# Optimization experiments

Hardware: AMD Instinct MI355X
Metric: run time of the kernel (lower is better)

## Reference

```python
import jax, jax.numpy as jnp
import numpy as np

A = 0.7071067811865476  # sqrt(2)/2
B_ = 1.0 - A
KH = KW = 3
K2 = 9
STRIDE = 1
PAD = 1
DIL = 1


def setup_inputs() -> dict:
    key = jax.random.key(0)
    k1, k2, k3, k4 = jax.random.split(key, 4)
    Bn, Cin, H, W = 4, 256, 64, 64
    Cout = 256
    x = jax.random.normal(k1, (Bn, Cin, H, W), dtype=jnp.float32)
    offset = jax.random.normal(k2, (Bn, 2 * K2, H, W), dtype=jnp.float32)
    mask = jax.random.uniform(k3, (Bn, K2, H, W), dtype=jnp.float32)
    stdv = 1.0 / np.sqrt(Cin * KH * KW)
    weight = jax.random.uniform(k4, (Cout, Cin, KH, KW), dtype=jnp.float32,
                                minval=-stdv, maxval=stdv)
    bias = jnp.zeros((Cout,), dtype=jnp.float32)
    return {"input": x, "offset": offset, "mask": mask, "weight": weight, "bias": bias}


def _weight_circle(weight):
    # Blend 3x3 corner taps along the diagonal "circle", as in DCNv2_Circle.forward.
    O, C = weight.shape[0], weight.shape[1]
    w = weight.reshape(O, C, K2)
    w0 = A * (A * w[:, :, 0] + B_ * w[:, :, 1]) + B_ * (A * w[:, :, 3] + B_ * w[:, :, 4])
    w2 = A * (B_ * w[:, :, 1] + A * w[:, :, 2]) + B_ * (B_ * w[:, :, 4] + A * w[:, :, 5])
    w6 = B_ * (A * w[:, :, 3] + B_ * w[:, :, 4]) + A * (A * w[:, :, 6] + B_ * w[:, :, 7])
    w8 = B_ * (B_ * w[:, :, 4] + A * w[:, :, 5]) + A * (B_ * w[:, :, 7] + A * w[:, :, 8])
    return jnp.stack([w0, w[:, :, 1], w2, w[:, :, 3], w[:, :, 4],
                      w[:, :, 5], w6, w[:, :, 7], w8], axis=-1)  # [O, C, 9]


def _dcn_v2(x, offset, mask, w_flat, bias):
    Bn, C, H, W = x.shape
    Ho = (H + 2 * PAD - DIL * (KH - 1) - 1) // STRIDE + 1
    Wo = (W + 2 * PAD - DIL * (KW - 1) - 1) // STRIDE + 1
    # Base sampling grid per kernel tap k: [K2, Ho, Wo]
    ki, kj = jnp.meshgrid(jnp.arange(KH), jnp.arange(KW), indexing="ij")
    ki = ki.reshape(K2).astype(jnp.float32)
    kj = kj.reshape(K2).astype(jnp.float32)
    oy = (jnp.arange(Ho, dtype=jnp.float32) * STRIDE - PAD)
    ox = (jnp.arange(Wo, dtype=jnp.float32) * STRIDE - PAD)
    base_y = oy[None, :, None] + DIL * ki[:, None, None]  # [K2, Ho, 1]
    base_x = ox[None, None, :] + DIL * kj[:, None, None]  # [K2, 1, Wo]
    # Offsets: channel 2k is dy, 2k+1 is dx (DCNv2 layout).
    off = offset.reshape(Bn, K2, 2, Ho, Wo)
    y = base_y[None] + off[:, :, 0]  # [B, K2, Ho, Wo]
    x_ = base_x[None] + off[:, :, 1]
    y0 = jnp.floor(y)
    x0 = jnp.floor(x_)
    ly = y - y0
    lx = x_ - x0
    y0i = y0.astype(jnp.int32)
    x0i = x0.astype(jnp.int32)
    flat = x.reshape(Bn, C, H * W)

    def gather(yi, xi):
        valid = (yi >= 0) & (yi < H) & (xi >= 0) & (xi < W)
        idx = jnp.clip(yi, 0, H - 1) * W + jnp.clip(xi, 0, W - 1)  # [B,K2,Ho,Wo]
        v = jax.vmap(lambda f, i: f[:, i.reshape(-1)])(flat, idx)  # [B,C,K2*Ho*Wo]
        v = v.reshape(Bn, C, K2, Ho, Wo)
        return v * valid[:, None].astype(v.dtype)

    hy = 1.0 - ly
    hx = 1.0 - lx
    # corner weights broadcast over channel dim
    sampled = (gather(y0i, x0i) * (hy * hx)[:, None]
               + gather(y0i, x0i + 1) * (hy * lx)[:, None]
               + gather(y0i + 1, x0i) * (ly * hx)[:, None]
               + gather(y0i + 1, x0i + 1) * (ly * lx)[:, None])  # [B,C,K2,Ho,Wo]
    sampled = sampled * mask[:, None]  # modulation
    out = jnp.einsum("bckhw,ock->bohw", sampled, w_flat)
    return out + bias[None, :, None, None]


def reference(input, offset, mask, weight, bias):
    w_flat = _weight_circle(weight)
    return _dcn_v2(input, offset, mask, w_flat, bias)
```

## Files before the change

kernel.cpp:

```cpp
#include <hip/hip_runtime.h>

typedef __bf16 bf16x8 __attribute__((ext_vector_type(8)));
typedef float f32x4 __attribute__((ext_vector_type(4)));

#define HH 64
#define WW 64
#define HW 4096
#define COUT 256
#define NROWS 12
#define XS_OFF 37888
#define SMEM_SZ 65536

__device__ __forceinline__ void bar_sync() {
    asm volatile("s_waitcnt lgkmcnt(0)" ::: "memory");
    __builtin_amdgcn_s_barrier();
    asm volatile("" ::: "memory");
}
__device__ __forceinline__ void bar_sync_vm() {
    asm volatile("s_waitcnt vmcnt(0) lgkmcnt(0)" ::: "memory");
    __builtin_amdgcn_s_barrier();
    asm volatile("" ::: "memory");
}

__global__ __launch_bounds__(256) void prep_weights(const float* __restrict__ weight,
                                                    __bf16* __restrict__ wp) {
    __shared__ float ws[2304];
    const int o = blockIdx.x;
    const int tid = threadIdx.x;
    const float4* src = (const float4*)(weight + (size_t)o * 2304);
    float4* dst = (float4*)ws;
    #pragma unroll
    for (int i = 0; i < 3; ++i) {
        int idx = i * 256 + tid;
        if (idx < 576) dst[idx] = src[idx];
    }
    __syncthreads();
    const float Af = 0.70710678118654752f;
    const float Bf = 1.0f - Af;
    const int tm = o >> 4, rr = o & 15;
    for (int fid = tid; fid < 288; fid += 256) {
        const int cgtap = fid >> 2, q = fid & 3;
        const int cg = cgtap / 9, tap = cgtap - 9 * cg;
        const int c0 = cg * 32 + q * 8;
        bf16x8 v;
        #pragma unroll
        for (int j = 0; j < 8; ++j) {
            const float* w = ws + (c0 + j) * 9;
            float r;
            switch (tap) {
                case 0:  r = Af*(Af*w[0]+Bf*w[1]) + Bf*(Af*w[3]+Bf*w[4]); break;
                case 1:  r = w[1]; break;
                case 2:  r = Af*(Bf*w[1]+Af*w[2]) + Bf*(Bf*w[4]+Af*w[5]); break;
                case 3:  r = w[3]; break;
                case 4:  r = w[4]; break;
                case 5:  r = w[5]; break;
                case 6:  r = Bf*(Af*w[3]+Bf*w[4]) + Af*(Af*w[6]+Bf*w[7]); break;
                case 7:  r = w[7]; break;
                default: r = Bf*(Bf*w[4]+Af*w[5]) + Af*(Bf*w[7]+Af*w[8]); break;
            }
            v[j] = (__bf16)r;
        }
        *(bf16x8*)&wp[(size_t)(((cg * 9 + tap) * 16 + tm) * 64 + q * 16 + rr) << 3] = v;
    }
}

__global__ __launch_bounds__(256) void prep_x(const float* __restrict__ x,
                                              __bf16* __restrict__ xs) {
    __shared__ float lds[16384];
    const int bh = blockIdx.x;
    const int tid = threadIdx.x;
    const int b = bh >> 6, h = bh & 63;
    const int w4 = (tid & 15) * 4;
    const int cb = tid >> 4;
    #pragma unroll
    for (int it = 0; it < 16; ++it) {
        const int c = cb + it * 16;
        float4 v = *(const float4*)(x + ((size_t)(b * 256 + c)) * HW + h * 64 + w4);
        #pragma unroll
        for (int e = 0; e < 4; ++e) {
            int w = w4 + e;
            lds[w * 256 + (c ^ (w & 31))] = ((const float*)&v)[e];
        }
    }
    __syncthreads();
    #pragma unroll
    for (int it = 0; it < 8; ++it) {
        const int u = it * 256 + tid;
        const int gsg = u >> 6, w = u & 63;
        bf16x8 v;
        #pragma unroll
        for (int c8 = 0; c8 < 8; ++c8)
            v[c8] = (__bf16)lds[w * 256 + ((gsg * 8 + c8) ^ (w & 31))];
        *(bf16x8*)&xs[(size_t)bh * 16384 + (size_t)u * 8] = v;
    }
}

__global__ __launch_bounds__(512, 2) void dcn_main(
        const float* __restrict__ x, const float* __restrict__ off,
        const float* __restrict__ msk, const __bf16* __restrict__ wp,
        const __bf16* __restrict__ xs, const float* __restrict__ bias,
        float* __restrict__ out) {
    __shared__ __align__(16) char smem[SMEM_SZ];
    char* BsB = smem;
    const char* XsB = (const char*)smem + XS_OFF;

    const int tid  = threadIdx.x;
    const int wv   = tid >> 6;
    const int lane = tid & 63;
    const int q    = lane >> 4, rr = lane & 15;
    const int px   = lane;

    const int bid = blockIdx.x;
    const int xcd = bid & 7;
    const int b   = xcd >> 1;
    const int h   = ((xcd & 1) << 5) | (bid >> 3);

    const int rowbase = min(max(h - 5, 0), HH - NROWS);
    const float* xb = x + (size_t)b * 256 * HW;
    const char* xsb = (const char*)xs;

    size_t SB[3]; int XD[3];
    #pragma unroll
    for (int k = 0; k < 3; ++k) {
        int t = wv * 3 + k;
        int row = t >> 1, sgh = t & 1;
        SB[k] = (size_t)(b * 64 + rowbase + row) * 32768 + (size_t)(sgh * 1024 + lane * 16);
        XD[k] = XS_OFF + row * 2048 + sgh * 1024;
    }

    float W00[3], W01[3], W10[3], W11[3];
    int AY0[3], AY1[3], DXO[3], COLB[3], GP[3];
    bool UV[3];
    #pragma unroll
    for (int k = 0; k < 3; ++k) {
        int c = (k < 2) ? (wv + 8 * k) : ((wv >= 6) ? wv + 10 : -1);
        UV[k] = (c >= 0);
        if (UV[k]) {
            int sg = c / 9, tap = c % 9;
            int ki = tap / 3, kj = tap - 3 * ki;
            const float* offp = off + (size_t)b * 18 * HW + h * 64 + px;
            float dy = offp[(2 * tap) * HW];
            float dx = offp[(2 * tap + 1) * HW];
            float mv = msk[(size_t)b * 9 * HW + (size_t)tap * HW + h * 64 + px];
            float py  = (float)(h - 1 + ki) + dy;
            float pxf = (float)(px - 1 + kj) + dx;
            float y0f = floorf(py), x0f = floorf(pxf);
            float ly = py - y0f, lx = pxf - x0f;
            float hy = 1.0f - ly, hx = 1.0f - lx;
            int y0 = (int)y0f, x0 = (int)x0f;
            int y1 = y0 + 1, x1 = x0 + 1;
            bool vy0 = (y0 >= 0) && (y0 < HH), vy1 = (y1 >= 0) && (y1 < HH);
            bool vx0 = (x0 >= 0) && (x0 < WW), vx1 = (x1 >= 0) && (x1 < WW);
            int cy0 = min(max(y0, 0), HH - 1), cy1 = min(max(y1, 0), HH - 1);
            int cx0 = min(max(x0, 0), WW - 1), cx1 = min(max(x1, 0), WW - 1);
            W00[k] = (vy0 && vx0) ? hy * hx * mv : 0.0f;
            W01[k] = (vy0 && vx1) ? hy * lx * mv : 0.0f;
            W10[k] = (vy1 && vx0) ? ly * hx * mv : 0.0f;
            W11[k] = (vy1 && vx1) ? ly * lx * mv : 0.0f;
            int ry0 = min(max(cy0 - rowbase, 0), NROWS - 1);
            int ry1 = min(max(cy1 - rowbase, 0), NROWS - 1);
            bool useG = (vy0 && (cy0 < rowbase || cy0 > rowbase + NROWS - 1))
                     || (vy1 && (cy1 < rowbase || cy1 > rowbase + NROWS - 1));
            AY0[k]  = ry0 * 2048 + sg * 1024 + cx0 * 16;
            AY1[k]  = ry1 * 2048 + sg * 1024 + cx0 * 16;
            DXO[k]  = (cx1 - cx0) * 16;
            COLB[k] = (tap * 32 + sg * 8) * 2;
            GP[k]   = cy0 | (cy1 << 6) | (cx0 << 12) | (cx1 << 18) | (sg << 24)
                    | (useG ? (1u << 31) : 0);
        }
    }

    f32x4 acc[4][4];
    #pragma unroll
    for (int i = 0; i < 4; ++i)
        #pragma unroll
        for (int n = 0; n < 4; ++n)
            acc[i][n] = (f32x4)0.0f;

    const int tm0   = (wv & 3) * 4;
    const int klbeg = (wv & 4) ? 5 : 0;
    const int nkl   = (wv & 4) ? 4 : 5;

    #pragma unroll
    for (int k = 0; k < 3; ++k)
        __builtin_amdgcn_global_load_lds(
            (const __attribute__((address_space(1))) void*)(xsb + SB[k]),
            (__attribute__((address_space(3))) void*)(smem + XD[k]), 16, 0, 0);

    #pragma unroll 1
    for (int s = 0; s < 16; ++s) {
        const int cg = s >> 1, half = s & 1;
        bar_sync_vm();
        #pragma unroll
        for (int k = 0; k < 3; ++k) {
            if (UV[k]) {
                bf16x8 c00 = *(const bf16x8*)(XsB + AY0[k]);
                bf16x8 c01 = *(const bf16x8*)(XsB + AY0[k] + DXO[k]);
                bf16x8 c10 = *(const bf16x8*)(XsB + AY1[k]);
                bf16x8 c11 = *(const bf16x8*)(XsB + AY1[k] + DXO[k]);
                float w0 = W00[k], w1 = W01[k], w2 = W10[k], w3 = W11[k];
                bf16x8 res;
                #pragma unroll
                for (int j = 0; j < 8; ++j) {
                    float v = w0 * (float)c00[j] + w1 * (float)c01[j]
                            + w2 * (float)c10[j] + w3 * (float)c11[j];
                    res[j] = (__bf16)v;
                }
                int gp = GP[k];
                if (gp < 0) {
                    int cy0 = gp & 63, cy1 = (gp >> 6) & 63;
                    int cx0 = (gp >> 12) & 63, cx1 = (gp >> 18) & 63;
                    int sg = (gp >> 24) & 3;
                    const float* xc = xb + (size_t)(cg * 32 + half * 16 + sg * 8) * HW;
                    int i00 = cy0 * 64 + cx0, i01 = cy0 * 64 + cx1;
                    int i10 = cy1 * 64 + cx0, i11 = cy1 * 64 + cx1;
                    #pragma unroll
                    for (int j = 0; j < 8; ++j) {
                        float v = w0 * xc[i00] + w1 * xc[i01]
                                + w2 * xc[i10] + w3 * xc[i11];
                        res[j] = (__bf16)v;
                        xc += HW;
                    }
                }
                *(bf16x8*)(BsB + px * 592 + COLB[k] + half * 32) = res;
            }
        }
        bar_sync();
        if (s < 15) {
            #pragma unroll
            for (int k = 0; k < 3; ++k)
                __builtin_amdgcn_global_load_lds(
                    (const __attribute__((address_space(1))) void*)(xsb + SB[k] + (size_t)(s + 1) * 2048),
                    (__attribute__((address_space(3))) void*)(smem + XD[k]), 16, 0, 0);
        }
        if (half) {
            const __bf16* ap = wp + ((size_t)((cg * 9 + klbeg) * 16 + tm0) * 64 + lane) * 8;
            bf16x8 a0 = *(const bf16x8*)ap;
            bf16x8 a1 = *(const bf16x8*)(ap + 512);
            bf16x8 a2 = *(const bf16x8*)(ap + 1024);
            bf16x8 a3 = *(const bf16x8*)(ap + 1536);
            int kc = (klbeg * 32 + q * 8) * 2;
            #pragma unroll 1
            for (int t = 0; t < nkl; ++t) {
                bf16x8 n0 = a0, n1 = a1, n2 = a2, n3 = a3;
                if (t + 1 < nkl) {
                    const __bf16* np = ap + 8192;
                    n0 = *(const bf16x8*)np;
                    n1 = *(const bf16x8*)(np + 512);
                    n2 = *(const bf16x8*)(np + 1024);
                    n3 = *(const bf16x8*)(np + 1536);
                }
                const char* bp = BsB + rr * 592 + kc;
                bf16x8 bb0 = *(const bf16x8*)(bp);
                bf16x8 bb1 = *(const bf16x8*)(bp + 16 * 592);
                bf16x8 bb2 = *(const bf16x8*)(bp + 32 * 592);
                bf16x8 bb3 = *(const bf16x8*)(bp + 48 * 592);
                acc[0][0] = __builtin_amdgcn_mfma_f32_16x16x32_bf16(a0, bb0, acc[0][0], 0, 0, 0);
                acc[1][0] = __builtin_amdgcn_mfma_f32_16x16x32_bf16(a1, bb0, acc[1][0], 0, 0, 0);
                acc[2][0] = __builtin_amdgcn_mfma_f32_16x16x32_bf16(a2, bb0, acc[2][0], 0, 0, 0);
                acc[3][0] = __builtin_amdgcn_mfma_f32_16x16x32_bf16(a3, bb0, acc[3][0], 0, 0, 0);
                acc[0][1] = __builtin_amdgcn_mfma_f32_16x16x32_bf16(a0, bb1, acc[0][1], 0, 0, 0);
                acc[1][1] = __builtin_amdgcn_mfma_f32_16x16x32_bf16(a1, bb1, acc[1][1], 0, 0, 0);
                acc[2][1] = __builtin_amdgcn_mfma_f32_16x16x32_bf16(a2, bb1, acc[2][1], 0, 0, 0);
                acc[3][1] = __builtin_amdgcn_mfma_f32_16x16x32_bf16(a3, bb1, acc[3][1], 0, 0, 0);
                acc[0][2] = __builtin_amdgcn_mfma_f32_16x16x32_bf16(a0, bb2, acc[0][2], 0, 0, 0);
                acc[1][2] = __builtin_amdgcn_mfma_f32_16x16x32_bf16(a1, bb2, acc[1][2], 0, 0, 0);
                acc[2][2] = __builtin_amdgcn_mfma_f32_16x16x32_bf16(a2, bb2, acc[2][2], 0, 0, 0);
                acc[3][2] = __builtin_amdgcn_mfma_f32_16x16x32_bf16(a3, bb2, acc[3][2], 0, 0, 0);
                acc[0][3] = __builtin_amdgcn_mfma_f32_16x16x32_bf16(a0, bb3, acc[0][3], 0, 0, 0);
                acc[1][3] = __builtin_amdgcn_mfma_f32_16x16x32_bf16(a1, bb3, acc[1][3], 0, 0, 0);
                acc[2][3] = __builtin_amdgcn_mfma_f32_16x16x32_bf16(a2, bb3, acc[2][3], 0, 0, 0);
                acc[3][3] = __builtin_amdgcn_mfma_f32_16x16x32_bf16(a3, bb3, acc[3][3], 0, 0, 0);
                ap += 8192;
                kc += 64;
                a0 = n0; a1 = n1; a2 = n2; a3 = n3;
            }
        }
    }

    float* scr = (float*)smem;
    bar_sync();
    if (wv >= 4) {
        const int base = (wv - 4) * 4096 + lane * 4;
        #pragma unroll
        for (int i = 0; i < 4; ++i)
            #pragma unroll
            for (int n = 0; n < 4; ++n)
                *(f32x4*)&scr[base + (i * 4 + n) * 256] = acc[i][n];
    }
    bar_sync();
    if (wv < 4) {
        const int mrow = wv * 64;
        const int base = wv * 4096 + lane * 4;
        #pragma unroll
        for (int i = 0; i < 4; ++i) {
            #pragma unroll
            for (int n = 0; n < 4; ++n) {
                f32x4 p = *(const f32x4*)&scr[base + (i * 4 + n) * 256];
                #pragma unroll
                for (int e = 0; e < 4; ++e) {
                    int m = mrow + i * 16 + q * 4 + e;
                    out[((size_t)b * COUT + m) * HW + h * 64 + n * 16 + rr]
                        = acc[i][n][e] + p[e] + bias[m];
                }
            }
        }
    }
}

extern "C" void kernel_launch(void* const* d_in, const int* in_sizes, int n_in,
                              void* d_out, int out_size, void* d_ws, size_t ws_size,
                              hipStream_t stream) {
    const float* x      = (const float*)d_in[0];
    const float* off    = (const float*)d_in[1];
    const float* msk    = (const float*)d_in[2];
    const float* weight = (const float*)d_in[3];
    const float* bias   = (const float*)d_in[4];
    float* out = (float*)d_out;

    __bf16* wp = (__bf16*)d_ws;
    __bf16* xs = (__bf16*)((char*)d_ws + 1179648);

    prep_weights<<<256, 256, 0, stream>>>(weight, wp);
    prep_x<<<256, 256, 0, stream>>>(x, xs);
    dcn_main<<<256, 512, 0, stream>>>(x, off, msk, wp, xs, bias, out);
}
```

Baseline: 133.3 us.

## Merge prep kernels and prefetch weight fragments one stage ahead of MFMA

Combines the weight-prep and x-prep kernels into one launch with 512 blocks. The x transpose now reads global memory directly instead of going through an LDS transpose. In the main kernel, the A (weight) fragments for a whole channel group are loaded into registers during the even half-step, so their latency overlaps the bilinear sampling. The MFMA loop is fully unrolled. This saves a launch and hides global-load latency, at the cost of many more VGPRs (20 bf16x8 fragments) under launch_bounds(512,2), which risks spills. The x-prep reads are now strided and uncoalesced.

```diff
diff --git a/kernel.cpp b/kernel.cpp
--- a/kernel.cpp
+++ b/kernel.cpp
@@ -22,11 +22,29 @@
     asm volatile("" ::: "memory");
 }
 
-__global__ __launch_bounds__(256) void prep_weights(const float* __restrict__ weight,
-                                                    __bf16* __restrict__ wp) {
+__global__ __launch_bounds__(256) void prep(const float* __restrict__ weight,
+                                            const float* __restrict__ x,
+                                            __bf16* __restrict__ wp,
+                                            __bf16* __restrict__ xs) {
     __shared__ float ws[2304];
-    const int o = blockIdx.x;
     const int tid = threadIdx.x;
+    if (blockIdx.x < 256) {
+        const int bh = blockIdx.x;
+        const int b = bh >> 6, h = bh & 63;
+        const float* xr = x + (size_t)b * 256 * HW + h * 64;
+        #pragma unroll
+        for (int it = 0; it < 8; ++it) {
+            const int u = it * 256 + tid;
+            const int gsg = u >> 6, w = u & 63;
+            bf16x8 v;
+            #pragma unroll
+            for (int c8 = 0; c8 < 8; ++c8)
+                v[c8] = (__bf16)xr[(size_t)(gsg * 8 + c8) * HW + w];
+            *(bf16x8*)&xs[(size_t)bh * 16384 + (size_t)u * 8] = v;
+        }
+        return;
+    }
+    const int o = blockIdx.x - 256;
     const float4* src = (const float4*)(weight + (size_t)o * 2304);
     float4* dst = (float4*)ws;
     #pragma unroll
@@ -61,37 +79,6 @@
             v[j] = (__bf16)r;
         }
         *(bf16x8*)&wp[(size_t)(((cg * 9 + tap) * 16 + tm) * 64 + q * 16 + rr) << 3] = v;
-    }
-}
-
-__global__ __launch_bounds__(256) void prep_x(const float* __restrict__ x,
-                                              __bf16* __restrict__ xs) {
-    __shared__ float lds[16384];
-    const int bh = blockIdx.x;
-    const int tid = threadIdx.x;
-    const int b = bh >> 6, h = bh & 63;
-    const int w4 = (tid & 15) * 4;
-    const int cb = tid >> 4;
-    #pragma unroll
-    for (int it = 0; it < 16; ++it) {
-        const int c = cb + it * 16;
-        float4 v = *(const float4*)(x + ((size_t)(b * 256 + c)) * HW + h * 64 + w4);
-        #pragma unroll
-        for (int e = 0; e < 4; ++e) {
-            int w = w4 + e;
-            lds[w * 256 + (c ^ (w & 31))] = ((const float*)&v)[e];
-        }
-    }
-    __syncthreads();
-    #pragma unroll
-    for (int it = 0; it < 8; ++it) {
-        const int u = it * 256 + tid;
-        const int gsg = u >> 6, w = u & 63;
-        bf16x8 v;
-        #pragma unroll
-        for (int c8 = 0; c8 < 8; ++c8)
-            v[c8] = (__bf16)lds[w * 256 + ((gsg * 8 + c8) ^ (w & 31))];
-        *(bf16x8*)&xs[(size_t)bh * 16384 + (size_t)u * 8] = v;
     }
 }
 
@@ -181,6 +168,8 @@
     const int klbeg = (wv & 4) ? 5 : 0;
     const int nkl   = (wv & 4) ? 4 : 5;
 
+    bf16x8 Afr[5][4];
+
     #pragma unroll
     for (int k = 0; k < 3; ++k)
         __builtin_amdgcn_global_load_lds(
@@ -191,6 +180,17 @@
     for (int s = 0; s < 16; ++s) {
         const int cg = s >> 1, half = s & 1;
         bar_sync_vm();
+        if (!half) {
+            const __bf16* ap = wp + ((size_t)((cg * 9 + klbeg) * 16 + tm0) * 64 + lane) * 8;
+            #pragma unroll
+            for (int t = 0; t < 5; ++t) {
+                if (t < nkl) {
+                    #pragma unroll
+                    for (int i = 0; i < 4; ++i)
+                        Afr[t][i] = *(const bf16x8*)(ap + t * 8192 + i * 512);
+                }
+            }
+        }
         #pragma unroll
         for (int k = 0; k < 3; ++k) {
             if (UV[k]) {
@@ -234,46 +234,32 @@
                     (__attribute__((address_space(3))) void*)(smem + XD[k]), 16, 0, 0);
         }
         if (half) {
-            const __bf16* ap = wp + ((size_t)((cg * 9 + klbeg) * 16 + tm0) * 64 + lane) * 8;
-            bf16x8 a0 = *(const bf16x8*)ap;
-            bf16x8 a1 = *(const bf16x8*)(ap + 512);
-            bf16x8 a2 = *(const bf16x8*)(ap + 1024);
-            bf16x8 a3 = *(const bf16x8*)(ap + 1536);
-            int kc = (klbeg * 32 + q * 8) * 2;
-            #pragma unroll 1
-            for (int t = 0; t < nkl; ++t) {
-                bf16x8 n0 = a0, n1 = a1, n2 = a2, n3 = a3;
-                if (t + 1 < nkl) {
-                    const __bf16* np = ap + 8192;
-                    n0 = *(const bf16x8*)np;
-                    n1 = *(const bf16x8*)(np + 512);
-                    n2 = *(const bf16x8*)(np + 1024);
-                    n3 = *(const bf16x8*)(np + 1536);
-                }
-                const char* bp = BsB + rr * 592 + kc;
-                bf16x8 bb0 = *(const bf16x8*)(bp);
-                bf16x8 bb1 = *(const bf16x8*)(bp + 16 * 592);
-                bf16x8 bb2 = *(const bf16x8*)(bp + 32 * 592);
-                bf16x8 bb3 = *(const bf16x8*)(bp + 48 * 592);
-                acc[0][0] = __builtin_amdgcn_mfma_f32_16x16x32_bf16(a0, bb0, acc[0][0], 0, 0, 0);
-                acc[1][0] = __builtin_amdgcn_mfma_f32_16x16x32_bf16(a1, bb0, acc[1][0], 0, 0, 0);
-                acc[2][0] = __builtin_amdgcn_mfma_f32_16x16x32_bf16(a2, bb0, acc[2][0], 0, 0, 0);
-                acc[3][0] = __builtin_amdgcn_mfma_f32_16x16x32_bf16(a3, bb0, acc[3][0], 0, 0, 0);
-                acc[0][1] = __builtin_amdgcn_mfma_f32_16x16x32_bf16(a0, bb1, acc[0][1], 0, 0, 0);
-                acc[1][1] = __builtin_amdgcn_mfma_f32_16x16x32_bf16(a1, bb1, acc[1][1], 0, 0, 0);
-                acc[2][1] = __builtin_amdgcn_mfma_f32_16x16x32_bf16(a2, bb1, acc[2][1], 0, 0, 0);
-                acc[3][1] = __builtin_amdgcn_mfma_f32_16x16x32_bf16(a3, bb1, acc[3][1], 0, 0, 0);
-                acc[0][2] = __builtin_amdgcn_mfma_f32_16x16x32_bf16(a0, bb2, acc[0][2], 0, 0, 0);
-                acc[1][2] = __builtin_amdgcn_mfma_f32_16x16x32_bf16(a1, bb2, acc[1][2], 0, 0, 0);
-                acc[2][2] = __builtin_amdgcn_mfma_f32_16x16x32_bf16(a2, bb2, acc[2][2], 0, 0, 0);
-                acc[3][2] = __builtin_amdgcn_mfma_f32_16x16x32_bf16(a3, bb2, acc[3][2], 0, 0, 0);
-                acc[0][3] = __builtin_amdgcn_mfma_f32_16x16x32_bf16(a0, bb3, acc[0][3], 0, 0, 0);
-                acc[1][3] = __builtin_amdgcn_mfma_f32_16x16x32_bf16(a1, bb3, acc[1][3], 0, 0, 0);
-                acc[2][3] = __builtin_amdgcn_mfma_f32_16x16x32_bf16(a2, bb3, acc[2][3], 0, 0, 0);
-                acc[3][3] = __builtin_amdgcn_mfma_f32_16x16x32_bf16(a3, bb3, acc[3][3], 0, 0, 0);
-                ap += 8192;
-                kc += 64;
-                a0 = n0; a1 = n1; a2 = n2; a3 = n3;
+            const char* bp0 = BsB + rr * 592 + (klbeg * 32 + q * 8) * 2;
+            #pragma unroll
+            for (int t = 0; t < 5; ++t) {
+                if (t < nkl) {
+                    const char* bp = bp0 + t * 64;
+                    bf16x8 bb0 = *(const bf16x8*)(bp);
+                    bf16x8 bb1 = *(const bf16x8*)(bp + 16 * 592);
+                    bf16x8 bb2 = *(const bf16x8*)(bp + 32 * 592);
+                    bf16x8 bb3 = *(const bf16x8*)(bp + 48 * 592);
+                    acc[0][0] = __builtin_amdgcn_mfma_f32_16x16x32_bf16(Afr[t][0], bb0, acc[0][0], 0, 0, 0);
+                    acc[1][0] = __builtin_amdgcn_mfma_f32_16x16x32_bf16(Afr[t][1], bb0, acc[1][0], 0, 0, 0);
+                    acc[2][0] = __builtin_amdgcn_mfma_f32_16x16x32_bf16(Afr[t][2], bb0, acc[2][0], 0, 0, 0);
+                    acc[3][0] = __builtin_amdgcn_mfma_f32_16x16x32_bf16(Afr[t][3], bb0, acc[3][0], 0, 0, 0);
+                    acc[0][1] = __builtin_amdgcn_mfma_f32_16x16x32_bf16(Afr[t][0], bb1, acc[0][1], 0, 0, 0);
+                    acc[1][1] = __builtin_amdgcn_mfma_f32_16x16x32_bf16(Afr[t][1], bb1, acc[1][1], 0, 0, 0);
+                    acc[2][1] = __builtin_amdgcn_mfma_f32_16x16x32_bf16(Afr[t][2], bb1, acc[2][1], 0, 0, 0);
+                    acc[3][1] = __builtin_amdgcn_mfma_f32_16x16x32_bf16(Afr[t][3], bb1, acc[3][1], 0, 0, 0);
+                    acc[0][2] = __builtin_amdgcn_mfma_f32_16x16x32_bf16(Afr[t][0], bb2, acc[0][2], 0, 0, 0);
+                    acc[1][2] = __builtin_amdgcn_mfma_f32_16x16x32_bf16(Afr[t][1], bb2, acc[1][2], 0, 0, 0);
+                    acc[2][2] = __builtin_amdgcn_mfma_f32_16x16x32_bf16(Afr[t][2], bb2, acc[2][2], 0, 0, 0);
+                    acc[3][2] = __builtin_amdgcn_mfma_f32_16x16x32_bf16(Afr[t][3], bb2, acc[3][2], 0, 0, 0);
+                    acc[0][3] = __builtin_amdgcn_mfma_f32_16x16x32_bf16(Afr[t][0], bb3, acc[0][3], 0, 0, 0);
+                    acc[1][3] = __builtin_amdgcn_mfma_f32_16x16x32_bf16(Afr[t][1], bb3, acc[1][3], 0, 0, 0);
+                    acc[2][3] = __builtin_amdgcn_mfma_f32_16x16x32_bf16(Afr[t][2], bb3, acc[2][3], 0, 0, 0);
+                    acc[3][3] = __builtin_amdgcn_mfma_f32_16x16x32_bf16(Afr[t][3], bb3, acc[3][3], 0, 0, 0);
+                }
             }
         }
     }
@@ -321,7 +307,6 @@
     __bf16* wp = (__bf16*)d_ws;
     __bf16* xs = (__bf16*)((char*)d_ws + 1179648);
 
-    prep_weights<<<256, 256, 0, stream>>>(weight, wp);
-    prep_x<<<256, 256, 0, stream>>>(x, xs);
+    prep<<<512, 256, 0, stream>>>(weight, x, wp, xs);
     dcn_main<<<256, 512, 0, stream>>>(x, off, msk, wp, xs, bias, out);
 }
```

After: 160.7 us. 1.21x slower.

## Double-buffer LDS to overlap bilinear sampling with MFMA, merge prep kernels

Applied to the files above, without the earlier changes.

The main loop now keeps two LDS buffers for both the staged input rows and the sampled B tile. It computes the MFMA for the previous channel group, split across the two half-steps, while the current group is being sampled, which drops one barrier per step. The two prep kernels are merged into a single launch, and the x transpose now reads global memory directly instead of going through LDS. LDS use grows to about 122KB per block, which removes any chance of two resident blocks per CU and adds a tail MFMA pass after the loop.

```diff
diff --git a/kernel.cpp b/kernel.cpp
--- a/kernel.cpp
+++ b/kernel.cpp
@@ -8,8 +8,10 @@
 #define HW 4096
 #define COUT 256
 #define NROWS 12
-#define XS_OFF 37888
-#define SMEM_SZ 65536
+#define BS_SZ 37888
+#define XS_OFF 75776
+#define XS_SZ 24576
+#define SMEM_SZ 124928
 
 __device__ __forceinline__ void bar_sync() {
     asm volatile("s_waitcnt lgkmcnt(0)" ::: "memory");
@@ -22,11 +24,29 @@
     asm volatile("" ::: "memory");
 }
 
-__global__ __launch_bounds__(256) void prep_weights(const float* __restrict__ weight,
-                                                    __bf16* __restrict__ wp) {
+__global__ __launch_bounds__(256) void prep(const float* __restrict__ weight,
+                                            const float* __restrict__ x,
+                                            __bf16* __restrict__ wp,
+                                            __bf16* __restrict__ xs) {
     __shared__ float ws[2304];
-    const int o = blockIdx.x;
     const int tid = threadIdx.x;
+    if (blockIdx.x < 256) {
+        const int bh = blockIdx.x;
+        const int b = bh >> 6, h = bh & 63;
+        const float* xr = x + (size_t)b * 256 * HW + h * 64;
+        #pragma unroll
+        for (int it = 0; it < 8; ++it) {
+            const int u = it * 256 + tid;
+            const int gsg = u >> 6, w = u & 63;
+            bf16x8 v;
+            #pragma unroll
+            for (int c8 = 0; c8 < 8; ++c8)
+                v[c8] = (__bf16)xr[(size_t)(gsg * 8 + c8) * HW + w];
+            *(bf16x8*)&xs[(size_t)bh * 16384 + (size_t)u * 8] = v;
+        }
+        return;
+    }
+    const int o = blockIdx.x - 256;
     const float4* src = (const float4*)(weight + (size_t)o * 2304);
     float4* dst = (float4*)ws;
     #pragma unroll
@@ -64,34 +84,49 @@
     }
 }
 
-__global__ __launch_bounds__(256) void prep_x(const float* __restrict__ x,
-                                              __bf16* __restrict__ xs) {
-    __shared__ float lds[16384];
-    const int bh = blockIdx.x;
-    const int tid = threadIdx.x;
-    const int b = bh >> 6, h = bh & 63;
-    const int w4 = (tid & 15) * 4;
-    const int cb = tid >> 4;
-    #pragma unroll
-    for (int it = 0; it < 16; ++it) {
-        const int c = cb + it * 16;
-        float4 v = *(const float4*)(x + ((size_t)(b * 256 + c)) * HW + h * 64 + w4);
-        #pragma unroll
-        for (int e = 0; e < 4; ++e) {
-            int w = w4 + e;
-            lds[w * 256 + (c ^ (w & 31))] = ((const float*)&v)[e];
-        }
-    }
-    __syncthreads();
-    #pragma unroll
-    for (int it = 0; it < 8; ++it) {
-        const int u = it * 256 + tid;
-        const int gsg = u >> 6, w = u & 63;
-        bf16x8 v;
-        #pragma unroll
-        for (int c8 = 0; c8 < 8; ++c8)
-            v[c8] = (__bf16)lds[w * 256 + ((gsg * 8 + c8) ^ (w & 31))];
-        *(bf16x8*)&xs[(size_t)bh * 16384 + (size_t)u * 8] = v;
+__device__ __forceinline__ void mfma_part(const __bf16* __restrict__ wp,
+        const char* BsR, int klbeg, int tb, int te, int tm0, int lane,
+        int q, int rr, int pcg, f32x4 acc[4][4]) {
+    const __bf16* ap = wp + ((size_t)((pcg * 9 + klbeg + tb) * 16 + tm0) * 64 + lane) * 8;
+    bf16x8 a0 = *(const bf16x8*)ap;
+    bf16x8 a1 = *(const bf16x8*)(ap + 512);
+    bf16x8 a2 = *(const bf16x8*)(ap + 1024);
+    bf16x8 a3 = *(const bf16x8*)(ap + 1536);
+    int kc = ((klbeg + tb) * 32 + q * 8) * 2;
+    #pragma unroll 1
+    for (int t = tb; t < te; ++t) {
+        bf16x8 n0 = a0, n1 = a1, n2 = a2, n3 = a3;
+        if (t + 1 < te) {
+            const __bf16* np = ap + 8192;
+            n0 = *(const bf16x8*)np;
+            n1 = *(const bf16x8*)(np + 512);
+            n2 = *(const bf16x8*)(np + 1024);
+            n3 = *(const bf16x8*)(np + 1536);
+        }
+        const char* bp = BsR + rr * 592 + kc;
+        bf16x8 bb0 = *(const bf16x8*)(bp);
+        bf16x8 bb1 = *(const bf16x8*)(bp + 16 * 592);
+        bf16x8 bb2 = *(const bf16x8*)(bp + 32 * 592);
+        bf16x8 bb3 = *(const bf16x8*)(bp + 48 * 592);
+        acc[0][0] = __builtin_amdgcn_mfma_f32_16x16x32_bf16(a0, bb0, acc[0][0], 0, 0, 0);
+        acc[1][0] = __builtin_amdgcn_mfma_f32_16x16x32_bf16(a1, bb0, acc[1][0], 0, 0, 0);
+        acc[2][0] = __builtin_amdgcn_mfma_f32_16x16x32_bf16(a2, bb0, acc[2][0], 0, 0, 0);
+        acc[3][0] = __builtin_amdgcn_mfma_f32_16x16x32_bf16(a3, bb0, acc[3][0], 0, 0, 0);
+        acc[0][1] = __builtin_amdgcn_mfma_f32_16x16x32_bf16(a0, bb1, acc[0][1], 0, 0, 0);
+        acc[1][1] = __builtin_amdgcn_mfma_f32_16x16x32_bf16(a1, bb1, acc[1][1], 0, 0, 0);
+        acc[2][1] = __builtin_amdgcn_mfma_f32_16x16x32_bf16(a2, bb1, acc[2][1], 0, 0, 0);
+        acc[3][1] = __builtin_amdgcn_mfma_f32_16x16x32_bf16(a3, bb1, acc[3][1], 0, 0, 0);
+        acc[0][2] = __builtin_amdgcn_mfma_f32_16x16x32_bf16(a0, bb2, acc[0][2], 0, 0, 0);
+        acc[1][2] = __builtin_amdgcn_mfma_f32_16x16x32_bf16(a1, bb2, acc[1][2], 0, 0, 0);
+        acc[2][2] = __builtin_amdgcn_mfma_f32_16x16x32_bf16(a2, bb2, acc[2][2], 0, 0, 0);
+        acc[3][2] = __builtin_amdgcn_mfma_f32_16x16x32_bf16(a3, bb2, acc[3][2], 0, 0, 0);
+        acc[0][3] = __builtin_amdgcn_mfma_f32_16x16x32_bf16(a0, bb3, acc[0][3], 0, 0, 0);
+        acc[1][3] = __builtin_amdgcn_mfma_f32_16x16x32_bf16(a1, bb3, acc[1][3], 0, 0, 0);
+        acc[2][3] = __builtin_amdgcn_mfma_f32_16x16x32_bf16(a2, bb3, acc[2][3], 0, 0, 0);
+        acc[3][3] = __builtin_amdgcn_mfma_f32_16x16x32_bf16(a3, bb3, acc[3][3], 0, 0, 0);
+        ap += 8192;
+        kc += 64;
+        a0 = n0; a1 = n1; a2 = n2; a3 = n3;
     }
 }
 
@@ -101,9 +136,6 @@
         const __bf16* __restrict__ xs, const float* __restrict__ bias,
         float* __restrict__ out) {
     __shared__ __align__(16) char smem[SMEM_SZ];
-    char* BsB = smem;
-    const char* XsB = (const char*)smem + XS_OFF;
-
     const int tid  = threadIdx.x;
     const int wv   = tid >> 6;
     const int lane = tid & 63;
@@ -119,13 +151,13 @@
     const float* xb = x + (size_t)b * 256 * HW;
     const char* xsb = (const char*)xs;
 
-    size_t SB[3]; int XD[3];
+    size_t SB[3]; int XDR[3];
     #pragma unroll
     for (int k = 0; k < 3; ++k) {
         int t = wv * 3 + k;
         int row = t >> 1, sgh = t & 1;
-        SB[k] = (size_t)(b * 64 + rowbase + row) * 32768 + (size_t)(sgh * 1024 + lane * 16);
-        XD[k] = XS_OFF + row * 2048 + sgh * 1024;
+        SB[k]  = (size_t)(b * 64 + rowbase + row) * 32768 + (size_t)(sgh * 1024 + lane * 16);
+        XDR[k] = row * 2048 + sgh * 1024;
     }
 
     float W00[3], W01[3], W10[3], W11[3];
@@ -180,103 +212,75 @@
     const int tm0   = (wv & 3) * 4;
     const int klbeg = (wv & 4) ? 5 : 0;
     const int nkl   = (wv & 4) ? 4 : 5;
+    const int thalf = (nkl + 1) >> 1;
 
     #pragma unroll
     for (int k = 0; k < 3; ++k)
         __builtin_amdgcn_global_load_lds(
             (const __attribute__((address_space(1))) void*)(xsb + SB[k]),
-            (__attribute__((address_space(3))) void*)(smem + XD[k]), 16, 0, 0);
+            (__attribute__((address_space(3))) void*)(smem + XS_OFF + XDR[k]), 16, 0, 0);
 
     #pragma unroll 1
     for (int s = 0; s < 16; ++s) {
         const int cg = s >> 1, half = s & 1;
         bar_sync_vm();
-        #pragma unroll
-        for (int k = 0; k < 3; ++k) {
-            if (UV[k]) {
-                bf16x8 c00 = *(const bf16x8*)(XsB + AY0[k]);
-                bf16x8 c01 = *(const bf16x8*)(XsB + AY0[k] + DXO[k]);
-                bf16x8 c10 = *(const bf16x8*)(XsB + AY1[k]);
-                bf16x8 c11 = *(const bf16x8*)(XsB + AY1[k] + DXO[k]);
-                float w0 = W00[k], w1 = W01[k], w2 = W10[k], w3 = W11[k];
-                bf16x8 res;
-                #pragma unroll
-                for (int j = 0; j < 8; ++j) {
-                    float v = w0 * (float)c00[j] + w1 * (float)c01[j]
-                            + w2 * (float)c10[j] + w3 * (float)c11[j];
-                    res[j] = (__bf16)v;
-                }
-                int gp = GP[k];
-                if (gp < 0) {
-                    int cy0 = gp & 63, cy1 = (gp >> 6) & 63;
-                    int cx0 = (gp >> 12) & 63, cx1 = (gp >> 18) & 63;
-                    int sg = (gp >> 24) & 3;
-                    const float* xc = xb + (size_t)(cg * 32 + half * 16 + sg * 8) * HW;
-                    int i00 = cy0 * 64 + cx0, i01 = cy0 * 64 + cx1;
-                    int i10 = cy1 * 64 + cx0, i11 = cy1 * 64 + cx1;
-                    #pragma unroll
-                    for (int j = 0; j < 8; ++j) {
-                        float v = w0 * xc[i00] + w1 * xc[i01]
-                                + w2 * xc[i10] + w3 * xc[i11];
-                        res[j] = (__bf16)v;
-                        xc += HW;
-                    }
-                }
-                *(bf16x8*)(BsB + px * 592 + COLB[k] + half * 32) = res;
-            }
-        }
-        bar_sync();
         if (s < 15) {
+            const int xoff = XS_OFF + ((s + 1) & 1) * XS_SZ;
             #pragma unroll
             for (int k = 0; k < 3; ++k)
                 __builtin_amdgcn_global_load_lds(
                     (const __attribute__((address_space(1))) void*)(xsb + SB[k] + (size_t)(s + 1) * 2048),
-                    (__attribute__((address_space(3))) void*)(smem + XD[k]), 16, 0, 0);
-        }
-        if (half) {
-            const __bf16* ap = wp + ((size_t)((cg * 9 + klbeg) * 16 + tm0) * 64 + lane) * 8;
-            bf16x8 a0 = *(const bf16x8*)ap;
-            bf16x8 a1 = *(const bf16x8*)(ap + 512);
-            bf16x8 a2 = *(const bf16x8*)(ap + 1024);
-            bf16x8 a3 = *(const bf16x8*)(ap + 1536);
-            int kc = (klbeg * 32 + q * 8) * 2;
-            #pragma unroll 1
-            for (int t = 0; t < nkl; ++t) {
-                bf16x8 n0 = a0, n1 = a1, n2 = a2, n3 = a3;
-                if (t + 1 < nkl) {
-                    const __bf16* np = ap + 8192;
-                    n0 = *(const bf16x8*)np;
-                    n1 = *(const bf16x8*)(np + 512);
-                    n2 = *(const bf16x8*)(np + 1024);
-                    n3 = *(const bf16x8*)(np + 1536);
+                    (__attribute__((address_space(3))) void*)(smem + xoff + XDR[k]), 16, 0, 0);
+        }
+        {
+            const char* XsB = (const char*)smem + XS_OFF + (s & 1) * XS_SZ;
+            char* BsW = smem + (cg & 1) * BS_SZ;
+            #pragma unroll
+            for (int k = 0; k < 3; ++k) {
+                if (UV[k]) {
+                    bf16x8 c00 = *(const bf16x8*)(XsB + AY0[k]);
+                    bf16x8 c01 = *(const bf16x8*)(XsB + AY0[k] + DXO[k]);
+                    bf16x8 c10 = *(const bf16x8*)(XsB + AY1[k]);
+                    bf16x8 c11 = *(const bf16x8*)(XsB + AY1[k] + DXO[k]);
+                    float w0 = W00[k], w1 = W01[k], w2 = W10[k], w3 = W11[k];
+                    bf16x8 res;
+                    #pragma unroll
+                    for (int j = 0; j < 8; ++j) {
+                        float v = w0 * (float)c00[j] + w1 * (float)c01[j]
+                                + w2 * (float)c10[j] + w3 * (float)c11[j];
+                        res[j] = (__bf16)v;
+                    }
+                    int gp = GP[k];
+                    if (gp < 0) {
+                        int cy0 = gp & 63, cy1 = (gp >> 6) & 63;
+                        int cx0 = (gp >> 12) & 63, cx1 = (gp >> 18) & 63;
+                        int sg = (gp >> 24) & 3;
+                        const float* xc = xb + (size_t)(cg * 32 + half * 16 + sg * 8) * HW;
+                        int i00 = cy0 * 64 + cx0, i01 = cy0 * 64 + cx1;
+                        int i10 = cy1 * 64 + cx0, i11 = cy1 * 64 + cx1;
+                        #pragma unroll
+                        for (int j = 0; j < 8; ++j) {
+                            float v = w0 * xc[i00] + w1 * xc[i01]
+                                    + w2 * xc[i10] + w3 * xc[i11];
+                            res[j] = (__bf16)v;
+                            xc += HW;
+                        }
+                    }
+                    *(bf16x8*)(BsW + px * 592 + COLB[k] + half * 32) = res;
                 }
-                const char* bp = BsB + rr * 592 + kc;
-                bf16x8 bb0 = *(const bf16x8*)(bp);
-                bf16x8 bb1 = *(const bf16x8*)(bp + 16 * 592);
-                bf16x8 bb2 = *(const bf16x8*)(bp + 32 * 592);
-                bf16x8 bb3 = *(const bf16x8*)(bp + 48 * 592);
-                acc[0][0] = __builtin_amdgcn_mfma_f32_16x16x32_bf16(a0, bb0, acc[0][0], 0, 0, 0);
-                acc[1][0] = __builtin_amdgcn_mfma_f32_16x16x32_bf16(a1, bb0, acc[1][0], 0, 0, 0);
-                acc[2][0] = __builtin_amdgcn_mfma_f32_16x16x32_bf16(a2, bb0, acc[2][0], 0, 0, 0);
-                acc[3][0] = __builtin_amdgcn_mfma_f32_16x16x32_bf16(a3, bb0, acc[3][0], 0, 0, 0);
-                acc[0][1] = __builtin_amdgcn_mfma_f32_16x16x32_bf16(a0, bb1, acc[0][1], 0, 0, 0);
-                acc[1][1] = __builtin_amdgcn_mfma_f32_16x16x32_bf16(a1, bb1, acc[1][1], 0, 0, 0);
-                acc[2][1] = __builtin_amdgcn_mfma_f32_16x16x32_bf16(a2, bb1, acc[2][1], 0, 0, 0);
-                acc[3][1] = __builtin_amdgcn_mfma_f32_16x16x32_bf16(a3, bb1, acc[3][1], 0, 0, 0);
-                acc[0][2] = __builtin_amdgcn_mfma_f32_16x16x32_bf16(a0, bb2, acc[0][2], 0, 0, 0);
-                acc[1][2] = __builtin_amdgcn_mfma_f32_16x16x32_bf16(a1, bb2, acc[1][2], 0, 0, 0);
-                acc[2][2] = __builtin_amdgcn_mfma_f32_16x16x32_bf16(a2, bb2, acc[2][2], 0, 0, 0);
-                acc[3][2] = __builtin_amdgcn_mfma_f32_16x16x32_bf16(a3, bb2, acc[3][2], 0, 0, 0);
-                acc[0][3] = __builtin_amdgcn_mfma_f32_16x16x32_bf16(a0, bb3, acc[0][3], 0, 0, 0);
-                acc[1][3] = __builtin_amdgcn_mfma_f32_16x16x32_bf16(a1, bb3, acc[1][3], 0, 0, 0);
-                acc[2][3] = __builtin_amdgcn_mfma_f32_16x16x32_bf16(a2, bb3, acc[2][3], 0, 0, 0);
-                acc[3][3] = __builtin_amdgcn_mfma_f32_16x16x32_bf16(a3, bb3, acc[3][3], 0, 0, 0);
-                ap += 8192;
-                kc += 64;
-                a0 = n0; a1 = n1; a2 = n2; a3 = n3;
             }
         }
-    }
+        if (s >= 2) {
+            const int pcg = cg - 1;
+            const char* BsR = (const char*)smem + (pcg & 1) * BS_SZ;
+            const int tb = half ? thalf : 0;
+            const int te = half ? nkl : thalf;
+            mfma_part(wp, BsR, klbeg, tb, te, tm0, lane, q, rr, pcg, acc);
+        }
+    }
+
+    bar_sync();
+    mfma_part(wp, (const char*)smem + BS_SZ, klbeg, 0, nkl, tm0, lane, q, rr, 7, acc);
 
     float* scr = (float*)smem;
     bar_sync();
@@ -321,7 +325,6 @@
     __bf16* wp = (__bf16*)d_ws;
     __bf16* xs = (__bf16*)((char*)d_ws + 1179648);
 
-    prep_weights<<<256, 256, 0, stream>>>(weight, wp);
-    prep_x<<<256, 256, 0, stream>>>(x, xs);
+    prep<<<512, 256, 0, stream>>>(weight, x, wp, xs);
     dcn_main<<<256, 512, 0, stream>>>(x, off, msk, wp, xs, bias, out);
 }
```

Result: faster. 127.6 us (-4.3%).
